# Kernel optimization log

Hardware: AMD Instinct MI355X
Metric: run time of the kernel (lower is better)

Reference implementation:

```python
import jax, jax.numpy as jnp
import numpy as np

B, N_MM, N_V, N_A = 2, 256, 64, 128
DIM, HEADS, ATTN_RATIO, MLP_RATIO = 1024, 16, 0.25, 4.0
INNER = int(DIM * ATTN_RATIO)          # 256
HID = int(DIM * MLP_RATIO)             # 4096
SCALE = (DIM // HEADS) ** -0.5         # faithful to source: uses dim//num_heads
EPS = 1e-5


def setup_inputs() -> dict:
    key = jax.random.key(0)
    ks = jax.random.split(key, 16)
    s = 0.02
    return {
        "xmm": jax.random.normal(ks[0], (B, N_MM, DIM), jnp.float32),
        "xv": jax.random.normal(ks[1], (B, N_V, DIM), jnp.float32),
        "xa": jax.random.normal(ks[2], (B, N_A, DIM), jnp.float32),
        "ln_mm_w": jnp.ones((DIM,), jnp.float32),
        "ln_mm_b": jnp.zeros((DIM,), jnp.float32),
        "ln_v_w": jnp.ones((DIM,), jnp.float32),
        "ln_v_b": jnp.zeros((DIM,), jnp.float32),
        "ln_a_w": jnp.ones((DIM,), jnp.float32),
        "ln_a_b": jnp.zeros((DIM,), jnp.float32),
        "Wq": jax.random.normal(ks[3], (DIM, INNER), jnp.float32) * s,
        "Wkv": jax.random.normal(ks[4], (2 * DIM, 2 * INNER), jnp.float32) * s,
        "Wproj": jax.random.normal(ks[5], (INNER, DIM), jnp.float32) * s,
        "bproj": jnp.zeros((DIM,), jnp.float32),
        "ln_mlp_w": jnp.ones((DIM,), jnp.float32),
        "ln_mlp_b": jnp.zeros((DIM,), jnp.float32),
        "W1": jax.random.normal(ks[6], (DIM, HID), jnp.float32) * s,
        "b1": jnp.zeros((HID,), jnp.float32),
        "W2": jax.random.normal(ks[7], (HID, DIM), jnp.float32) * s,
        "b2": jnp.zeros((DIM,), jnp.float32),
    }


def _ln(x, w, b):
    m = x.mean(-1, keepdims=True)
    v = ((x - m) ** 2).mean(-1, keepdims=True)
    return (x - m) / jnp.sqrt(v + EPS) * w + b


def reference(xmm, xv, xa, ln_mm_w, ln_mm_b, ln_v_w, ln_v_b, ln_a_w, ln_a_b,
              Wq, Wkv, Wproj, bproj, ln_mlp_w, ln_mlp_b, W1, b1, W2, b2):
    hd = INNER // HEADS
    src_mm = _ln(xmm, ln_mm_w, ln_mm_b)
    src_v = _ln(xv, ln_v_w, ln_v_b)
    src_a = _ln(xa, ln_a_w, ln_a_b)

    # kv(x_va) where x_va = cat([xv broadcast over N_a, xa broadcast over N_v], -1).
    # Equivalent to projecting each stream separately and broadcast-adding:
    kv_v = src_v @ Wkv[:DIM]            # [B, N_v, 2*INNER]
    kv_a = src_a @ Wkv[DIM:]            # [B, N_a, 2*INNER]
    kv = kv_v[:, :, None, :] + kv_a[:, None, :, :]          # [B, N_v, N_a, 2*INNER]
    kv = kv.reshape(B, N_V * N_A, 2, HEADS, hd)
    k = kv[:, :, 0].transpose(0, 2, 1, 3)                   # [B, H, N_va, hd]
    v = kv[:, :, 1].transpose(0, 2, 1, 3)

    q = (src_mm @ Wq).reshape(B, N_MM, HEADS, hd).transpose(0, 2, 1, 3)

    attn = jnp.einsum('bhqd,bhkd->bhqk', q, k) * SCALE
    attn = jax.nn.softmax(attn, axis=-1)
    out = jnp.einsum('bhqk,bhkd->bhqd', attn, v)
    out = out.transpose(0, 2, 1, 3).reshape(B, N_MM, INNER)
    out = out @ Wproj + bproj

    xmm = xmm + out
    h = _ln(xmm, ln_mlp_w, ln_mlp_b)
    h = jax.nn.gelu(h @ W1 + b1, approximate=False) @ W2 + b2
    return xmm + h
```

## Files before the change

kernel.cpp:

```cpp
#include <hip/hip_runtime.h>
#include <hip/hip_bf16.h>
#include <math.h>


typedef unsigned short ushort_t;
typedef __attribute__((ext_vector_type(8))) __bf16 bf16x8;
typedef __attribute__((ext_vector_type(4))) float f32x4;

#define DEVFN static __device__ __forceinline__

DEVFN float bf2f(ushort_t u) {
    return __uint_as_float(((unsigned int)u) << 16);
}
DEVFN ushort_t f2bf(float f) {
    unsigned int x = __float_as_uint(f);
    unsigned int r = x + 0x7FFFu + ((x >> 16) & 1u);
    return (ushort_t)(r >> 16);
}
DEVFN void unpack8(uint4 dv, float* dst) {
    unsigned int ws[4] = {dv.x, dv.y, dv.z, dv.w};
#pragma unroll
    for (int i = 0; i < 4; i++) {
        dst[2 * i] = __uint_as_float(ws[i] << 16);
        dst[2 * i + 1] = __uint_as_float(ws[i] & 0xFFFF0000u);
    }
}

struct LNSeg {
    const float* x; const float* w; const float* b; ushort_t* out; int start;
};
struct TDesc { const float* in; ushort_t* out; int R, C, nx, start; };

__global__ __launch_bounds__(256) void prep_kernel(LNSeg l0, LNSeg l1,
                                                   LNSeg l2, TDesc d0,
                                                   TDesc d1, TDesc d2,
                                                   TDesc d3, TDesc d4,
                                                   float* stats) {
    int id = blockIdx.x;
    int tid = threadIdx.x;
    if (id == 0) ((float4*)stats)[tid] = (float4){0.f, 0.f, 0.f, 0.f};

    if (id < 896) {
        const float *x, *w, *b; ushort_t* o; int start;
        if (id >= l2.start)      { x = l2.x; w = l2.w; b = l2.b; o = l2.out; start = l2.start; }
        else if (id >= l1.start) { x = l1.x; w = l1.w; b = l1.b; o = l1.out; start = l1.start; }
        else                     { x = l0.x; w = l0.w; b = l0.b; o = l0.out; start = 0; }
        int row = id - start;
        const float4* xr4 = (const float4*)(x + (size_t)row * 1024);
        float4 v4 = xr4[tid];
        float s = v4.x + v4.y + v4.z + v4.w;
        float ss = v4.x * v4.x + v4.y * v4.y + v4.z * v4.z + v4.w * v4.w;
#pragma unroll
        for (int off = 32; off > 0; off >>= 1) {
            s += __shfl_down(s, off);
            ss += __shfl_down(ss, off);
        }
        __shared__ float red[8];
        if ((tid & 63) == 0) {
            red[tid >> 6] = s;
            red[4 + (tid >> 6)] = ss;
        }
        __syncthreads();
        s = red[0] + red[1] + red[2] + red[3];
        ss = red[4] + red[5] + red[6] + red[7];
        float mean = s * (1.f / 1024.f);
        float var = ss * (1.f / 1024.f) - mean * mean;
        float rstd = rsqrtf(var + 1e-5f);
        const float4 w4 = ((const float4*)w)[tid];
        const float4 b4 = ((const float4*)b)[tid];
        union { ushort_t u[4]; uint2 v; } pk;
        pk.u[0] = f2bf((v4.x - mean) * rstd * w4.x + b4.x);
        pk.u[1] = f2bf((v4.y - mean) * rstd * w4.y + b4.y);
        pk.u[2] = f2bf((v4.z - mean) * rstd * w4.z + b4.z);
        pk.u[3] = f2bf((v4.w - mean) * rstd * w4.w + b4.w);
        *(uint2*)(o + (size_t)row * 1024 + tid * 4) = pk.v;
        return;
    }

    int t = id - 896;
    const float* in; ushort_t* out; int R, C, nx, start;
    if (t >= d4.start)      { in = d4.in; out = d4.out; R = d4.R; C = d4.C; nx = d4.nx; start = d4.start; }
    else if (t >= d3.start) { in = d3.in; out = d3.out; R = d3.R; C = d3.C; nx = d3.nx; start = d3.start; }
    else if (t >= d2.start) { in = d2.in; out = d2.out; R = d2.R; C = d2.C; nx = d2.nx; start = d2.start; }
    else if (t >= d1.start) { in = d1.in; out = d1.out; R = d1.R; C = d1.C; nx = d1.nx; start = d1.start; }
    else                    { in = d0.in; out = d0.out; R = d0.R; C = d0.C; nx = d0.nx; start = 0; }
    int tt = t - start;
    int bx = (tt % nx) * 32;
    int by = (tt / nx) * 32;
    __shared__ ushort_t tile[32 * 33];
    int r = tid >> 3, c4 = (tid & 7) * 4;
    float4 f = *(const float4*)(in + (size_t)(by + r) * C + bx + c4);
    ushort_t* tr = tile + r * 33 + c4;
    tr[0] = f2bf(f.x); tr[1] = f2bf(f.y); tr[2] = f2bf(f.z); tr[3] = f2bf(f.w);
    __syncthreads();
    int oc = tid >> 3, or4 = (tid & 7) * 4;
    union { ushort_t u[4]; uint2 v; } pk;
#pragma unroll
    for (int j = 0; j < 4; j++) pk.u[j] = tile[(or4 + j) * 33 + oc];
    *(uint2*)(out + (size_t)(bx + oc) * R + by + or4) = pk.v;
}

template <int EPI, typename OutT>
DEVFN void gemm_item(const ushort_t* __restrict__ A, int lda,
                     const ushort_t* __restrict__ B, int ldb,
                     OutT* __restrict__ C, int ldc, int K, int m0, int n0,
                     ushort_t* As, ushort_t* Bs) {
    constexpr int LS = 40;
    int tid = threadIdx.x;
    int wave = tid >> 6, lane = tid & 63;
    int wm = wave >> 1, wn = wave & 1;
    int quad = lane >> 4, l16 = lane & 15;

    f32x4 acc[2][2];
#pragma unroll
    for (int i = 0; i < 2; i++)
#pragma unroll
        for (int j = 0; j < 2; j++) acc[i][j] = (f32x4){0.f, 0.f, 0.f, 0.f};

    int r = tid >> 2, c = tid & 3;
    const ushort_t* Ap = A + (size_t)(m0 + r) * lda + c * 8;
    const ushort_t* Bp = B + (size_t)(n0 + r) * ldb + c * 8;
    uint4 ra = *(const uint4*)Ap;
    uint4 rb = *(const uint4*)Bp;

    for (int k0 = 0; k0 < K; k0 += 32) {
        *(uint4*)(&As[r * LS + c * 8]) = ra;
        *(uint4*)(&Bs[r * LS + c * 8]) = rb;
        __syncthreads();
        if (k0 + 32 < K) {
            ra = *(const uint4*)(Ap + k0 + 32);
            rb = *(const uint4*)(Bp + k0 + 32);
        }
        bf16x8 af[2], bfr[2];
#pragma unroll
        for (int i = 0; i < 2; i++)
            af[i] = *(const bf16x8*)(&As[(wm * 32 + i * 16 + l16) * LS + quad * 8]);
#pragma unroll
        for (int j = 0; j < 2; j++)
            bfr[j] = *(const bf16x8*)(&Bs[(wn * 32 + j * 16 + l16) * LS + quad * 8]);
#pragma unroll
        for (int i = 0; i < 2; i++)
#pragma unroll
            for (int j = 0; j < 2; j++)
                acc[i][j] = __builtin_amdgcn_mfma_f32_16x16x32_bf16(
                    af[i], bfr[j], acc[i][j], 0, 0, 0);
        __syncthreads();
    }

#pragma unroll
    for (int i = 0; i < 2; i++)
#pragma unroll
        for (int j = 0; j < 2; j++) {
            int col = n0 + wn * 32 + j * 16 + l16;
            int rbase = m0 + wm * 32 + i * 16 + quad * 4;
#pragma unroll
            for (int rr = 0; rr < 4; rr++) {
                int row = rbase + rr;
                float vv = acc[i][j][rr];
                if constexpr (EPI == 5)
                    atomicAdd(&C[(size_t)row * ldc + col], vv);
                else
                    C[(size_t)row * ldc + col] = (OutT)f2bf(vv);
            }
        }
}

struct GSeg {
    const ushort_t* A; const ushort_t* B; ushort_t* C;
    int lda, ldb, ldc, nx, start;
};
__global__ __launch_bounds__(256) void gemm64_multi(GSeg s0, GSeg s1, GSeg s2,
                                                    int K) {
    __shared__ ushort_t As[64 * 40];
    __shared__ ushort_t Bs[64 * 40];
    int id = blockIdx.x;
    GSeg s = (id >= s2.start) ? s2 : ((id >= s1.start) ? s1 : s0);
    int t = id - s.start;
    gemm_item<0, ushort_t>(s.A, s.lda, s.B, s.ldb, s.C, s.ldc, K,
                           (t / s.nx) * 64, (t % s.nx) * 64, As, Bs);
}

__global__ __launch_bounds__(256) void gemm_mlp2(const ushort_t* __restrict__ g,
                                                 const ushort_t* __restrict__ W2t,
                                                 float* __restrict__ outp) {
    __shared__ ushort_t As[64 * 40];
    __shared__ ushort_t Bs[64 * 40];
    int z = blockIdx.z;
    gemm_item<5, float>(g + z * 1024, 4096, W2t + z * 1024, 4096, outp, 1024,
                        1024, blockIdx.y * 64, blockIdx.x * 64, As, Bs);
}

__global__ __launch_bounds__(256) void gemm_proj(
    const ushort_t* __restrict__ A, const ushort_t* __restrict__ Bt,
    const float* __restrict__ bproj, const float* __restrict__ xmm,
    const float* __restrict__ b2, float* __restrict__ y,
    float* __restrict__ outp, float* __restrict__ stats) {
    constexpr int LS = 40;
    __shared__ ushort_t As[64 * LS];
    __shared__ ushort_t Bs[64 * LS];
    int tid = threadIdx.x;
    int wave = tid >> 6, lane = tid & 63;
    int wm = wave >> 1, wn = wave & 1;
    int quad = lane >> 4, l16 = lane & 15;
    int m0 = blockIdx.y * 64, n0 = blockIdx.x * 64;

    f32x4 acc[2][2];
#pragma unroll
    for (int i = 0; i < 2; i++)
#pragma unroll
        for (int j = 0; j < 2; j++) acc[i][j] = (f32x4){0.f, 0.f, 0.f, 0.f};

    int r = tid >> 2, c = tid & 3;
    const ushort_t* Ap = A + (size_t)(m0 + r) * 256 + c * 8;
    const ushort_t* Bp = Bt + (size_t)(n0 + r) * 256 + c * 8;
    uint4 ra = *(const uint4*)Ap;
    uint4 rb = *(const uint4*)Bp;

    for (int k0 = 0; k0 < 256; k0 += 32) {
        *(uint4*)(&As[r * LS + c * 8]) = ra;
        *(uint4*)(&Bs[r * LS + c * 8]) = rb;
        __syncthreads();
        if (k0 + 32 < 256) {
            ra = *(const uint4*)(Ap + k0 + 32);
            rb = *(const uint4*)(Bp + k0 + 32);
        }
        bf16x8 af[2], bfr[2];
#pragma unroll
        for (int i = 0; i < 2; i++)
            af[i] = *(const bf16x8*)(&As[(wm * 32 + i * 16 + l16) * LS + quad * 8]);
#pragma unroll
        for (int j = 0; j < 2; j++)
            bfr[j] = *(const bf16x8*)(&Bs[(wn * 32 + j * 16 + l16) * LS + quad * 8]);
#pragma unroll
        for (int i = 0; i < 2; i++)
#pragma unroll
            for (int j = 0; j < 2; j++)
                acc[i][j] = __builtin_amdgcn_mfma_f32_16x16x32_bf16(
                    af[i], bfr[j], acc[i][j], 0, 0, 0);
        __syncthreads();
    }

    float rs[2][4] = {{0.f, 0.f, 0.f, 0.f}, {0.f, 0.f, 0.f, 0.f}};
    float rq[2][4] = {{0.f, 0.f, 0.f, 0.f}, {0.f, 0.f, 0.f, 0.f}};
#pragma unroll
    for (int i = 0; i < 2; i++)
#pragma unroll
        for (int j = 0; j < 2; j++) {
            int col = n0 + wn * 32 + j * 16 + l16;
            int rbase = m0 + wm * 32 + i * 16 + quad * 4;
            float bv = bproj[col];
            float b2v = b2[col];
#pragma unroll
            for (int rr = 0; rr < 4; rr++) {
                int row = rbase + rr;
                float vv = acc[i][j][rr] + bv + xmm[(size_t)row * 1024 + col];
                y[(size_t)row * 1024 + col] = vv;
                outp[(size_t)row * 1024 + col] = vv + b2v;
                rs[i][rr] += vv;
                rq[i][rr] += vv * vv;
            }
        }
#pragma unroll
    for (int i = 0; i < 2; i++)
#pragma unroll
        for (int rr = 0; rr < 4; rr++) {
            float s = rs[i][rr], q = rq[i][rr];
            s += __shfl_xor(s, 1); q += __shfl_xor(q, 1);
            s += __shfl_xor(s, 2); q += __shfl_xor(q, 2);
            s += __shfl_xor(s, 4); q += __shfl_xor(q, 4);
            s += __shfl_xor(s, 8); q += __shfl_xor(q, 8);
            if (l16 == 0) {
                int row = m0 + wm * 32 + i * 16 + quad * 4 + rr;
                atomicAdd(&stats[row], s);
                atomicAdd(&stats[512 + row], q);
            }
        }
}

__global__ __launch_bounds__(256) void gemm_mlp1(
    const float* __restrict__ y, const float* __restrict__ lnw,
    const float* __restrict__ lnb, const float* __restrict__ stats,
    const ushort_t* __restrict__ W1t, const float* __restrict__ b1,
    ushort_t* __restrict__ g) {
    constexpr int LS = 40;
    __shared__ ushort_t As[64 * LS];
    __shared__ ushort_t Bs[64 * LS];
    int tid = threadIdx.x;
    int wave = tid >> 6, lane = tid & 63;
    int wm = wave >> 1, wn = wave & 1;
    int quad = lane >> 4, l16 = lane & 15;
    int m0 = blockIdx.y * 64, n0 = blockIdx.x * 64;

    f32x4 acc[2][2];
#pragma unroll
    for (int i = 0; i < 2; i++)
#pragma unroll
        for (int j = 0; j < 2; j++) acc[i][j] = (f32x4){0.f, 0.f, 0.f, 0.f};

    int r = tid >> 2, c = tid & 3;
    int rowm = m0 + r;
    float s = stats[rowm], ss = stats[512 + rowm];
    float mean = s * (1.f / 1024.f);
    float rstd = rsqrtf(ss * (1.f / 1024.f) - mean * mean + 1e-5f);

    const float* yp = y + (size_t)rowm * 1024 + c * 8;
    const float* wp = lnw + c * 8;
    const float* bp = lnb + c * 8;
    const ushort_t* Bp = W1t + (size_t)(n0 + r) * 1024 + c * 8;
    float4 y0 = *(const float4*)yp, y1 = *(const float4*)(yp + 4);
    float4 w0 = *(const float4*)wp, w1 = *(const float4*)(wp + 4);
    float4 b0 = *(const float4*)bp, b1v = *(const float4*)(bp + 4);
    uint4 rb = *(const uint4*)Bp;

    for (int k0 = 0; k0 < 1024; k0 += 32) {
        union { ushort_t u[8]; uint4 v; } pa;
        pa.u[0] = f2bf((y0.x - mean) * rstd * w0.x + b0.x);
        pa.u[1] = f2bf((y0.y - mean) * rstd * w0.y + b0.y);
        pa.u[2] = f2bf((y0.z - mean) * rstd * w0.z + b0.z);
        pa.u[3] = f2bf((y0.w - mean) * rstd * w0.w + b0.w);
        pa.u[4] = f2bf((y1.x - mean) * rstd * w1.x + b1v.x);
        pa.u[5] = f2bf((y1.y - mean) * rstd * w1.y + b1v.y);
        pa.u[6] = f2bf((y1.z - mean) * rstd * w1.z + b1v.z);
        pa.u[7] = f2bf((y1.w - mean) * rstd * w1.w + b1v.w);
        *(uint4*)(&As[r * LS + c * 8]) = pa.v;
        *(uint4*)(&Bs[r * LS + c * 8]) = rb;
        __syncthreads();
        if (k0 + 32 < 1024) {
            y0 = *(const float4*)(yp + k0 + 32);
            y1 = *(const float4*)(yp + k0 + 36);
            w0 = *(const float4*)(wp + k0 + 32);
            w1 = *(const float4*)(wp + k0 + 36);
            b0 = *(const float4*)(bp + k0 + 32);
            b1v = *(const float4*)(bp + k0 + 36);
            rb = *(const uint4*)(Bp + k0 + 32);
        }
        bf16x8 af[2], bfr[2];
#pragma unroll
        for (int i = 0; i < 2; i++)
            af[i] = *(const bf16x8*)(&As[(wm * 32 + i * 16 + l16) * LS + quad * 8]);
#pragma unroll
        for (int j = 0; j < 2; j++)
            bfr[j] = *(const bf16x8*)(&Bs[(wn * 32 + j * 16 + l16) * LS + quad * 8]);
#pragma unroll
        for (int i = 0; i < 2; i++)
#pragma unroll
            for (int j = 0; j < 2; j++)
                acc[i][j] = __builtin_amdgcn_mfma_f32_16x16x32_bf16(
                    af[i], bfr[j], acc[i][j], 0, 0, 0);
        __syncthreads();
    }

#pragma unroll
    for (int i = 0; i < 2; i++)
#pragma unroll
        for (int j = 0; j < 2; j++) {
            int col = n0 + wn * 32 + j * 16 + l16;
            int rbase = m0 + wm * 32 + i * 16 + quad * 4;
            float bv = b1[col];
#pragma unroll
            for (int rr = 0; rr < 4; rr++) {
                int row = rbase + rr;
                float vv = acc[i][j][rr] + bv;
                vv = 0.5f * vv * (1.f + erff(vv * 0.70710678118654752f));
                g[(size_t)row * 4096 + col] = f2bf(vv);
            }
        }
}

__global__ __launch_bounds__(256) void attn_kernel(
    const ushort_t* __restrict__ q, const ushort_t* __restrict__ kvv,
    const ushort_t* __restrict__ kva, ushort_t* __restrict__ out) {
    int bh = blockIdx.x;
    int b = bh >> 4, h = bh & 15;
    int tid = threadIdx.x;

    __shared__ float Kv[64][16], Vv[64][16], Ka[128][16], Va[128][16];
    {
        int row = tid >> 2, seg = (tid >> 1) & 1, half = tid & 1;
        const ushort_t* src =
            kvv + (size_t)(b * 64 + row) * 512 + seg * 256 + h * 16 + half * 8;
        float* dst = (seg ? Vv[row] : Kv[row]) + half * 8;
        unpack8(*(const uint4*)src, dst);
    }
#pragma unroll
    for (int t2 = 0; t2 < 2; t2++) {
        int t = tid + t2 * 256;
        int row = t >> 2, seg = (t >> 1) & 1, half = t & 1;
        const ushort_t* src =
            kva + (size_t)(b * 128 + row) * 512 + seg * 256 + h * 16 + half * 8;
        float* dst = (seg ? Va[row] : Ka[row]) + half * 8;
        unpack8(*(const uint4*)src, dst);
    }
    __syncthreads();

    int qlocal = tid >> 2;
    int dg = tid & 3;
    int qrow = blockIdx.y * 64 + qlocal;
    const ushort_t* qp = q + (size_t)(b * 256 + qrow) * 256 + h * 16 + dg * 4;
    uint2 qu = *(const uint2*)qp;
    float4 qv;
    qv.x = __uint_as_float(qu.x << 16) * 0.125f;
    qv.y = __uint_as_float(qu.x & 0xFFFF0000u) * 0.125f;
    qv.z = __uint_as_float(qu.y << 16) * 0.125f;
    qv.w = __uint_as_float(qu.y & 0xFFFF0000u) * 0.125f;

    const float4* Kv4 = (const float4*)Kv;
    const float4* Vv4 = (const float4*)Vv;
    const float4* Ka4 = (const float4*)Ka;
    const float4* Va4 = (const float4*)Va;

    float4 ov = {0.f, 0.f, 0.f, 0.f};
    float den = 0.f;
#pragma unroll 8
    for (int i = 0; i < 64; i++) {
        float4 kk = Kv4[i * 4 + dg];
        float part = qv.x * kk.x + qv.y * kk.y + qv.z * kk.z + qv.w * kk.w;
        part += __shfl_xor(part, 1);
        part += __shfl_xor(part, 2);
        float pe = __expf(part);
        den += pe;
        float4 vv = Vv4[i * 4 + dg];
        ov.x += pe * vv.x; ov.y += pe * vv.y;
        ov.z += pe * vv.z; ov.w += pe * vv.w;
    }
    float4 oa = {0.f, 0.f, 0.f, 0.f};
    float dena = 0.f;
#pragma unroll 8
    for (int i = 0; i < 128; i++) {
        float4 kk = Ka4[i * 4 + dg];
        float part = qv.x * kk.x + qv.y * kk.y + qv.z * kk.z + qv.w * kk.w;
        part += __shfl_xor(part, 1);
        part += __shfl_xor(part, 2);
        float pe = __expf(part);
        dena += pe;
        float4 vv = Va4[i * 4 + dg];
        oa.x += pe * vv.x; oa.y += pe * vv.y;
        oa.z += pe * vv.z; oa.w += pe * vv.w;
    }

    float rv = 1.f / den, ra = 1.f / dena;
    union { ushort_t u[4]; uint2 v; } pk;
    pk.u[0] = f2bf(ov.x * rv + oa.x * ra);
    pk.u[1] = f2bf(ov.y * rv + oa.y * ra);
    pk.u[2] = f2bf(ov.z * rv + oa.z * ra);
    pk.u[3] = f2bf(ov.w * rv + oa.w * ra);
    *(uint2*)(out + (size_t)(b * 256 + qrow) * 256 + h * 16 + dg * 4) = pk.v;
}

extern "C" void kernel_launch(void* const* d_in, const int* in_sizes, int n_in,
                              void* d_out, int out_size, void* d_ws,
                              size_t ws_size, hipStream_t stream) {
    const float* xmm = (const float*)d_in[0];
    const float* xv = (const float*)d_in[1];
    const float* xa = (const float*)d_in[2];
    const float* ln_mm_w = (const float*)d_in[3];
    const float* ln_mm_b = (const float*)d_in[4];
    const float* ln_v_w = (const float*)d_in[5];
    const float* ln_v_b = (const float*)d_in[6];
    const float* ln_a_w = (const float*)d_in[7];
    const float* ln_a_b = (const float*)d_in[8];
    const float* Wq = (const float*)d_in[9];
    const float* Wkv = (const float*)d_in[10];
    const float* Wproj = (const float*)d_in[11];
    const float* bproj = (const float*)d_in[12];
    const float* ln_mlp_w = (const float*)d_in[13];
    const float* ln_mlp_b = (const float*)d_in[14];
    const float* W1 = (const float*)d_in[15];
    const float* b1 = (const float*)d_in[16];
    const float* W2 = (const float*)d_in[17];
    const float* b2 = (const float*)d_in[18];
    float* outp = (float*)d_out;

    char* w = (char*)d_ws;
    ushort_t* xmmN = (ushort_t*)w;    w += 512 * 1024 * 2;
    ushort_t* xvN = (ushort_t*)w;     w += 128 * 1024 * 2;
    ushort_t* xaN = (ushort_t*)w;     w += 256 * 1024 * 2;
    ushort_t* Wqt = (ushort_t*)w;     w += 256 * 1024 * 2;
    ushort_t* Wkvt = (ushort_t*)w;    w += 512 * 2048 * 2;
    ushort_t* Wprojt = (ushort_t*)w;  w += 1024 * 256 * 2;
    ushort_t* W1t = (ushort_t*)w;     w += 4096 * 1024 * 2;
    ushort_t* W2t = (ushort_t*)w;     w += 1024 * 4096 * 2;
    ushort_t* qout = (ushort_t*)w;    w += 512 * 256 * 2;
    ushort_t* kvvb = (ushort_t*)w;    w += 128 * 512 * 2;
    ushort_t* kvab = (ushort_t*)w;    w += 256 * 512 * 2;
    ushort_t* attnout = (ushort_t*)w; w += 512 * 256 * 2;
    float* y = (float*)w;             w += 512 * 1024 * 4;
    ushort_t* g = (ushort_t*)w;       w += 512 * 4096 * 2;
    float* stats = (float*)w;         w += 1024 * 4;

    LNSeg L0{xmm, ln_mm_w, ln_mm_b, xmmN, 0};
    LNSeg L1{xv, ln_v_w, ln_v_b, xvN, 512};
    LNSeg L2{xa, ln_a_w, ln_a_b, xaN, 640};
    TDesc T0{Wq, Wqt, 1024, 256, 8, 0};
    TDesc T1{Wkv, Wkvt, 2048, 512, 16, 256};
    TDesc T2{Wproj, Wprojt, 256, 1024, 32, 1280};
    TDesc T3{W1, W1t, 1024, 4096, 128, 1536};
    TDesc T4{W2, W2t, 4096, 1024, 32, 5632};
    prep_kernel<<<896 + 9728, 256, 0, stream>>>(L0, L1, L2, T0, T1, T2, T3,
                                                T4, stats);

    GSeg G0{xmmN, Wqt, qout, 1024, 1024, 256, 4, 0};
    GSeg G1{xvN, Wkvt, kvvb, 1024, 2048, 512, 8, 32};
    GSeg G2{xaN, Wkvt + 1024, kvab, 1024, 2048, 512, 8, 48};
    gemm64_multi<<<80, 256, 0, stream>>>(G0, G1, G2, 1024);

    attn_kernel<<<dim3(32, 4), 256, 0, stream>>>(qout, kvvb, kvab, attnout);

    gemm_proj<<<dim3(16, 8), 256, 0, stream>>>(attnout, Wprojt, bproj, xmm,
                                               b2, y, outp, stats);

    gemm_mlp1<<<dim3(64, 8), 256, 0, stream>>>(y, ln_mlp_w, ln_mlp_b, stats,
                                               W1t, b1, g);

    gemm_mlp2<<<dim3(16, 8, 4), 256, 0, stream>>>(g, W2t, outp);

    (void)in_sizes; (void)n_in; (void)out_size; (void)ws_size;
}
```

Before: 204.9 us.

## Use 128x128 GEMM tiles for MLP and split LayerNorm into separate kernel

```diff
diff --git a/kernel.cpp b/kernel.cpp
--- a/kernel.cpp
+++ b/kernel.cpp
@@ -100,11 +100,10 @@
     *(uint2*)(out + (size_t)(bx + oc) * R + by + or4) = pk.v;
 }
 
-template <int EPI, typename OutT>
-DEVFN void gemm_item(const ushort_t* __restrict__ A, int lda,
-                     const ushort_t* __restrict__ B, int ldb,
-                     OutT* __restrict__ C, int ldc, int K, int m0, int n0,
-                     ushort_t* As, ushort_t* Bs) {
+DEVFN void gemm64_item(const ushort_t* __restrict__ A, int lda,
+                       const ushort_t* __restrict__ B, int ldb,
+                       ushort_t* __restrict__ C, int ldc, int K, int m0,
+                       int n0, ushort_t* As, ushort_t* Bs) {
     constexpr int LS = 40;
     int tid = threadIdx.x;
     int wave = tid >> 6, lane = tid & 63;
@@ -154,14 +153,8 @@
             int col = n0 + wn * 32 + j * 16 + l16;
             int rbase = m0 + wm * 32 + i * 16 + quad * 4;
 #pragma unroll
-            for (int rr = 0; rr < 4; rr++) {
-                int row = rbase + rr;
-                float vv = acc[i][j][rr];
-                if constexpr (EPI == 5)
-                    atomicAdd(&C[(size_t)row * ldc + col], vv);
-                else
-                    C[(size_t)row * ldc + col] = (OutT)f2bf(vv);
-            }
+            for (int rr = 0; rr < 4; rr++)
+                C[(size_t)(rbase + rr) * ldc + col] = f2bf(acc[i][j][rr]);
         }
 }
 
@@ -176,18 +169,104 @@
     int id = blockIdx.x;
     GSeg s = (id >= s2.start) ? s2 : ((id >= s1.start) ? s1 : s0);
     int t = id - s.start;
-    gemm_item<0, ushort_t>(s.A, s.lda, s.B, s.ldb, s.C, s.ldc, K,
-                           (t / s.nx) * 64, (t % s.nx) * 64, As, Bs);
-}
-
-__global__ __launch_bounds__(256) void gemm_mlp2(const ushort_t* __restrict__ g,
-                                                 const ushort_t* __restrict__ W2t,
-                                                 float* __restrict__ outp) {
-    __shared__ ushort_t As[64 * 40];
-    __shared__ ushort_t Bs[64 * 40];
+    gemm64_item(s.A, s.lda, s.B, s.ldb, s.C, s.ldc, K, (t / s.nx) * 64,
+                (t % s.nx) * 64, As, Bs);
+}
+
+template <int EPI, typename OutT>
+DEVFN void gemm128_core(const ushort_t* __restrict__ A, int lda,
+                        const ushort_t* __restrict__ B, int ldb,
+                        OutT* __restrict__ C, int ldc,
+                        const float* __restrict__ bias, int K, int m0, int n0,
+                        ushort_t* As, ushort_t* Bs) {
+    constexpr int LS = 40;
+    int tid = threadIdx.x;
+    int wave = tid >> 6, lane = tid & 63;
+    int wm = wave >> 1, wn = wave & 1;
+    int quad = lane >> 4, l16 = lane & 15;
+
+    f32x4 acc[4][4];
+#pragma unroll
+    for (int i = 0; i < 4; i++)
+#pragma unroll
+        for (int j = 0; j < 4; j++) acc[i][j] = (f32x4){0.f, 0.f, 0.f, 0.f};
+
+    int r = tid >> 1;
+    int c = (tid & 1) * 16;
+    const ushort_t* Ap = A + (size_t)(m0 + r) * lda + c;
+    const ushort_t* Bp = B + (size_t)(n0 + r) * ldb + c;
+    uint4 ra0 = *(const uint4*)Ap;
+    uint4 ra1 = *(const uint4*)(Ap + 8);
+    uint4 rb0 = *(const uint4*)Bp;
+    uint4 rb1 = *(const uint4*)(Bp + 8);
+
+    for (int k0 = 0; k0 < K; k0 += 32) {
+        *(uint4*)(&As[r * LS + c]) = ra0;
+        *(uint4*)(&As[r * LS + c + 8]) = ra1;
+        *(uint4*)(&Bs[r * LS + c]) = rb0;
+        *(uint4*)(&Bs[r * LS + c + 8]) = rb1;
+        __syncthreads();
+        if (k0 + 32 < K) {
+            ra0 = *(const uint4*)(Ap + k0 + 32);
+            ra1 = *(const uint4*)(Ap + k0 + 40);
+            rb0 = *(const uint4*)(Bp + k0 + 32);
+            rb1 = *(const uint4*)(Bp + k0 + 40);
+        }
+        bf16x8 af[4], bfr[4];
+#pragma unroll
+        for (int i = 0; i < 4; i++)
+            af[i] = *(const bf16x8*)(&As[(wm * 64 + i * 16 + l16) * LS + quad * 8]);
+#pragma unroll
+        for (int j = 0; j < 4; j++)
+            bfr[j] = *(const bf16x8*)(&Bs[(wn * 64 + j * 16 + l16) * LS + quad * 8]);
+#pragma unroll
+        for (int i = 0; i < 4; i++)
+#pragma unroll
+            for (int j = 0; j < 4; j++)
+                acc[i][j] = __builtin_amdgcn_mfma_f32_16x16x32_bf16(
+                    af[i], bfr[j], acc[i][j], 0, 0, 0);
+        __syncthreads();
+    }
+
+#pragma unroll
+    for (int i = 0; i < 4; i++)
+#pragma unroll
+        for (int j = 0; j < 4; j++) {
+            int col = n0 + wn * 64 + j * 16 + l16;
+            int rbase = m0 + wm * 64 + i * 16 + quad * 4;
+            float bv = (EPI == 2) ? bias[col] : 0.f;
+#pragma unroll
+            for (int rr = 0; rr < 4; rr++) {
+                int row = rbase + rr;
+                float vv = acc[i][j][rr] + bv;
+                if constexpr (EPI == 2) {
+                    vv = 0.5f * vv * (1.f + erff(vv * 0.70710678118654752f));
+                    C[(size_t)row * ldc + col] = (OutT)f2bf(vv);
+                } else {
+                    atomicAdd((float*)&C[(size_t)row * ldc + col], vv);
+                }
+            }
+        }
+}
+
+__global__ __launch_bounds__(256) void gemm_mlp1(
+    const ushort_t* __restrict__ h0, const ushort_t* __restrict__ W1t,
+    const float* __restrict__ b1, ushort_t* __restrict__ g) {
+    __shared__ ushort_t As[128 * 40];
+    __shared__ ushort_t Bs[128 * 40];
+    gemm128_core<2, ushort_t>(h0, 1024, W1t, 1024, g, 4096, b1, 1024,
+                              blockIdx.y * 128, blockIdx.x * 128, As, Bs);
+}
+
+__global__ __launch_bounds__(256) void gemm_mlp2(
+    const ushort_t* __restrict__ g, const ushort_t* __restrict__ W2t,
+    float* __restrict__ outp) {
+    __shared__ ushort_t As[128 * 40];
+    __shared__ ushort_t Bs[128 * 40];
     int z = blockIdx.z;
-    gemm_item<5, float>(g + z * 1024, 4096, W2t + z * 1024, 4096, outp, 1024,
-                        1024, blockIdx.y * 64, blockIdx.x * 64, As, Bs);
+    gemm128_core<5, float>(g + z * 512, 4096, W2t + z * 512, 4096, outp, 1024,
+                           nullptr, 512, blockIdx.y * 128, blockIdx.x * 128,
+                           As, Bs);
 }
 
 __global__ __launch_bounds__(256) void gemm_proj(
@@ -277,94 +356,23 @@
         }
 }
 
-__global__ __launch_bounds__(256) void gemm_mlp1(
-    const float* __restrict__ y, const float* __restrict__ lnw,
-    const float* __restrict__ lnb, const float* __restrict__ stats,
-    const ushort_t* __restrict__ W1t, const float* __restrict__ b1,
-    ushort_t* __restrict__ g) {
-    constexpr int LS = 40;
-    __shared__ ushort_t As[64 * LS];
-    __shared__ ushort_t Bs[64 * LS];
-    int tid = threadIdx.x;
-    int wave = tid >> 6, lane = tid & 63;
-    int wm = wave >> 1, wn = wave & 1;
-    int quad = lane >> 4, l16 = lane & 15;
-    int m0 = blockIdx.y * 64, n0 = blockIdx.x * 64;
-
-    f32x4 acc[2][2];
-#pragma unroll
-    for (int i = 0; i < 2; i++)
-#pragma unroll
-        for (int j = 0; j < 2; j++) acc[i][j] = (f32x4){0.f, 0.f, 0.f, 0.f};
-
-    int r = tid >> 2, c = tid & 3;
-    int rowm = m0 + r;
-    float s = stats[rowm], ss = stats[512 + rowm];
+__global__ __launch_bounds__(256) void ln_apply(
+    const float* __restrict__ y, const float* __restrict__ stats,
+    const float* __restrict__ w, const float* __restrict__ b,
+    ushort_t* __restrict__ h0) {
+    int row = blockIdx.x, tid = threadIdx.x;
+    float s = stats[row], ss = stats[512 + row];
     float mean = s * (1.f / 1024.f);
     float rstd = rsqrtf(ss * (1.f / 1024.f) - mean * mean + 1e-5f);
-
-    const float* yp = y + (size_t)rowm * 1024 + c * 8;
-    const float* wp = lnw + c * 8;
-    const float* bp = lnb + c * 8;
-    const ushort_t* Bp = W1t + (size_t)(n0 + r) * 1024 + c * 8;
-    float4 y0 = *(const float4*)yp, y1 = *(const float4*)(yp + 4);
-    float4 w0 = *(const float4*)wp, w1 = *(const float4*)(wp + 4);
-    float4 b0 = *(const float4*)bp, b1v = *(const float4*)(bp + 4);
-    uint4 rb = *(const uint4*)Bp;
-
-    for (int k0 = 0; k0 < 1024; k0 += 32) {
-        union { ushort_t u[8]; uint4 v; } pa;
-        pa.u[0] = f2bf((y0.x - mean) * rstd * w0.x + b0.x);
-        pa.u[1] = f2bf((y0.y - mean) * rstd * w0.y + b0.y);
-        pa.u[2] = f2bf((y0.z - mean) * rstd * w0.z + b0.z);
-        pa.u[3] = f2bf((y0.w - mean) * rstd * w0.w + b0.w);
-        pa.u[4] = f2bf((y1.x - mean) * rstd * w1.x + b1v.x);
-        pa.u[5] = f2bf((y1.y - mean) * rstd * w1.y + b1v.y);
-        pa.u[6] = f2bf((y1.z - mean) * rstd * w1.z + b1v.z);
-        pa.u[7] = f2bf((y1.w - mean) * rstd * w1.w + b1v.w);
-        *(uint4*)(&As[r * LS + c * 8]) = pa.v;
-        *(uint4*)(&Bs[r * LS + c * 8]) = rb;
-        __syncthreads();
-        if (k0 + 32 < 1024) {
-            y0 = *(const float4*)(yp + k0 + 32);
-            y1 = *(const float4*)(yp + k0 + 36);
-            w0 = *(const float4*)(wp + k0 + 32);
-            w1 = *(const float4*)(wp + k0 + 36);
-            b0 = *(const float4*)(bp + k0 + 32);
-            b1v = *(const float4*)(bp + k0 + 36);
-            rb = *(const uint4*)(Bp + k0 + 32);
-        }
-        bf16x8 af[2], bfr[2];
-#pragma unroll
-        for (int i = 0; i < 2; i++)
-            af[i] = *(const bf16x8*)(&As[(wm * 32 + i * 16 + l16) * LS + quad * 8]);
-#pragma unroll
-        for (int j = 0; j < 2; j++)
-            bfr[j] = *(const bf16x8*)(&Bs[(wn * 32 + j * 16 + l16) * LS + quad * 8]);
-#pragma unroll
-        for (int i = 0; i < 2; i++)
-#pragma unroll
-            for (int j = 0; j < 2; j++)
-                acc[i][j] = __builtin_amdgcn_mfma_f32_16x16x32_bf16(
-                    af[i], bfr[j], acc[i][j], 0, 0, 0);
-        __syncthreads();
-    }
-
-#pragma unroll
-    for (int i = 0; i < 2; i++)
-#pragma unroll
-        for (int j = 0; j < 2; j++) {
-            int col = n0 + wn * 32 + j * 16 + l16;
-            int rbase = m0 + wm * 32 + i * 16 + quad * 4;
-            float bv = b1[col];
-#pragma unroll
-            for (int rr = 0; rr < 4; rr++) {
-                int row = rbase + rr;
-                float vv = acc[i][j][rr] + bv;
-                vv = 0.5f * vv * (1.f + erff(vv * 0.70710678118654752f));
-                g[(size_t)row * 4096 + col] = f2bf(vv);
-            }
-        }
+    float4 v4 = ((const float4*)(y + (size_t)row * 1024))[tid];
+    float4 w4 = ((const float4*)w)[tid];
+    float4 b4 = ((const float4*)b)[tid];
+    union { ushort_t u[4]; uint2 v; } pk;
+    pk.u[0] = f2bf((v4.x - mean) * rstd * w4.x + b4.x);
+    pk.u[1] = f2bf((v4.y - mean) * rstd * w4.y + b4.y);
+    pk.u[2] = f2bf((v4.z - mean) * rstd * w4.z + b4.z);
+    pk.u[3] = f2bf((v4.w - mean) * rstd * w4.w + b4.w);
+    *(uint2*)(h0 + (size_t)row * 1024 + tid * 4) = pk.v;
 }
 
 __global__ __launch_bounds__(256) void attn_kernel(
@@ -485,6 +493,7 @@
     ushort_t* kvab = (ushort_t*)w;    w += 256 * 512 * 2;
     ushort_t* attnout = (ushort_t*)w; w += 512 * 256 * 2;
     float* y = (float*)w;             w += 512 * 1024 * 4;
+    ushort_t* h0 = (ushort_t*)w;      w += 512 * 1024 * 2;
     ushort_t* g = (ushort_t*)w;       w += 512 * 4096 * 2;
     float* stats = (float*)w;         w += 1024 * 4;
 
@@ -509,10 +518,11 @@
     gemm_proj<<<dim3(16, 8), 256, 0, stream>>>(attnout, Wprojt, bproj, xmm,
                                                b2, y, outp, stats);
 
-    gemm_mlp1<<<dim3(64, 8), 256, 0, stream>>>(y, ln_mlp_w, ln_mlp_b, stats,
-                                               W1t, b1, g);
-
-    gemm_mlp2<<<dim3(16, 8, 4), 256, 0, stream>>>(g, W2t, outp);
+    ln_apply<<<512, 256, 0, stream>>>(y, stats, ln_mlp_w, ln_mlp_b, h0);
+
+    gemm_mlp1<<<dim3(32, 4), 256, 0, stream>>>(h0, W1t, b1, g);
+
+    gemm_mlp2<<<dim3(8, 4, 8), 256, 0, stream>>>(g, W2t, outp);
 
     (void)in_sizes; (void)n_in; (void)out_size; (void)ws_size;
 }
```

Measured after the change: 213.9 us. 4.4% more time.
